# Performance work log

Measured on AMD Instinct MI355X. Metric: run time of the kernel, lower is better.

Reference implementation:

```python
import jax, jax.numpy as jnp
import numpy as np

NUM_HEADS = 16
HEAD_DIM = 64
MODEL_DIM = NUM_HEADS * HEAD_DIM  # 1024
N_TOKENS = 121
BATCH = 1024
DISTURB_HEADS = np.array([0, 3], dtype=int)


def setup_inputs() -> dict:
    key = jax.random.key(0)
    ks = jax.random.split(key, 8)
    scale = 1.0 / np.sqrt(MODEL_DIM)
    return {
        "query": jax.random.normal(ks[0], (BATCH, MODEL_DIM), dtype=jnp.float32),
        "key": jax.random.normal(ks[1], (BATCH, N_TOKENS, MODEL_DIM), dtype=jnp.float32),
        "value": jax.random.normal(ks[2], (BATCH, N_TOKENS, MODEL_DIM), dtype=jnp.float32),
        "Wq": jax.random.normal(ks[3], (MODEL_DIM, MODEL_DIM), dtype=jnp.float32) * scale,
        "bq": jnp.zeros((MODEL_DIM,), dtype=jnp.float32),
        "Wk": jax.random.normal(ks[4], (MODEL_DIM, MODEL_DIM), dtype=jnp.float32) * scale,
        "bk": jnp.zeros((MODEL_DIM,), dtype=jnp.float32),
        "Wv": jax.random.normal(ks[5], (MODEL_DIM, MODEL_DIM), dtype=jnp.float32) * scale,
        "bv": jnp.zeros((MODEL_DIM,), dtype=jnp.float32),
    }


def reference(query, key, value, Wq, bq, Wk, bk, Wv, bv):
    B, N, _ = key.shape
    H, d = NUM_HEADS, HEAD_DIM
    # Linear projections (plain GEMMs)
    q_proj = query @ Wq + bq            # [B, H*d]
    k_proj = key @ Wk + bk              # [B, N, H*d]
    v_proj = value @ Wv + bv            # [B, N, H*d]

    q = q_proj.reshape(B, H, d)         # [B, H, d]
    k = k_proj.reshape(B, N, H, d)      # [B, N, H, d]
    v = v_proj.reshape(B, N, H, d)

    # single-query scores per head: [B, H, N]
    scores = jnp.einsum('bhd,bnhd->bhn', q, k)
    # head-wise disturb override: masked heads get all-ones scores
    mask = jnp.zeros((H,), dtype=bool).at[DISTURB_HEADS].set(True)[None, :, None]
    scores = jnp.where(mask, jnp.ones_like(scores), scores)
    # note: original scales by sqrt(d * H), not sqrt(d)
    scores = scores / jnp.sqrt(jnp.asarray(d * H, dtype=scores.dtype))
    weights = jax.nn.softmax(scores, axis=-1)   # [B, H, N]
    output = jnp.einsum('bhn,bnhd->bhd', weights, v).reshape(B, H * d)
    return (output, weights)
```

## Files before the change

### kernel.cpp

```cpp
#include <hip/hip_runtime.h>
#include <hip/hip_bf16.h>

#define NHEADS 16
#define HDIM   64
#define MDIM   1024
#define NTOK   121
#define NBATCH 1024

typedef __attribute__((ext_vector_type(4))) float f32x4;
typedef __attribute__((ext_vector_type(4))) short s16x4;
typedef __attribute__((ext_vector_type(8))) short s16x8;

#define WAIT_VM(n)  asm volatile("s_waitcnt vmcnt(" #n ")" ::: "memory")
#define WAIT_LGKM0() asm volatile("s_waitcnt lgkmcnt(0)" ::: "memory")

__device__ __forceinline__ short f2bf(float f) {
  __hip_bfloat16 h = __float2bfloat16(f);
  return __builtin_bit_cast(short, h);
}

#define GLDS(gptr, lptr)                                                        \
  __builtin_amdgcn_global_load_lds(                                             \
      (const __attribute__((address_space(1))) void*)(gptr),                    \
      (__attribute__((address_space(3))) void*)(lptr), 16, 0, 0)

__global__ __launch_bounds__(256) void kTransW(const float* __restrict__ Wq,
                                               const float* __restrict__ Wk,
                                               const float* __restrict__ Wv,
                                               short* __restrict__ Wt) {
  int bid = blockIdx.x;
  int m = bid >> 8, tile = bid & 255;
  int tr = tile >> 4, tc = tile & 15;
  const float* W = (m == 0) ? Wq : (m == 1) ? Wk : Wv;
  short* T = Wt + (size_t)m * (MDIM * MDIM);
  __shared__ float tl[64][68];
  int t = threadIdx.x;
  int c4 = t & 15, r0 = t >> 4;
#pragma unroll
  for (int i = 0; i < 4; ++i) {
    int kr = r0 + i * 16;
    f32x4 v = *(const f32x4*)(W + (size_t)(tr * 64 + kr) * MDIM + tc * 64 + c4 * 4);
    *(f32x4*)&tl[kr][c4 * 4] = v;
  }
  __syncthreads();
#pragma unroll
  for (int i = 0; i < 4; ++i) {
    int n = r0 + i * 16;
    s16x4 o;
    o.x = f2bf(tl[c4 * 4 + 0][n]);
    o.y = f2bf(tl[c4 * 4 + 1][n]);
    o.z = f2bf(tl[c4 * 4 + 2][n]);
    o.w = f2bf(tl[c4 * 4 + 3][n]);
    *(s16x4*)(T + (size_t)(tc * 64 + n) * MDIM + tr * 64 + c4 * 4) = o;
  }
}

__device__ __forceinline__ void gemm_core(const float* __restrict__ A, int mrows,
                                          const short* __restrict__ Wt, int c0,
                                          short* Alds, short* Bl0, short* Bl1,
                                          f32x4 acc[4][4], int t) {
  int wid = t >> 6, lane = t & 63;
  int wr = wid >> 1, wc = wid & 1;
  int li = lane & 15, lg = lane >> 4;
  int kq = t & 15, r0s = t >> 4;
#pragma unroll
  for (int fm = 0; fm < 4; ++fm)
#pragma unroll
    for (int fn = 0; fn < 4; ++fn) acc[fm][fn] = (f32x4)0.0f;

  int rhi[4];
#pragma unroll
  for (int i = 0; i < 4; ++i) {
    int row = r0s + 64 + (i << 4);
    rhi[i] = row < mrows ? row : mrows - 1;
  }
#pragma unroll
  for (int i = 0; i < 4; ++i) {
    int cl = wid * 32 + i * 8 + (lane >> 3);
    int jg = (lane & 7) ^ (cl & 7);
    GLDS(Wt + (size_t)(c0 + cl) * MDIM + jg * 8, Bl0 + (wid * 32 + i * 8) * 64);
  }
  f32x4 rLo[4];
#pragma unroll
  for (int i = 0; i < 4; ++i)
    rLo[i] = *(const f32x4*)(A + (size_t)(r0s + (i << 4)) * MDIM + kq * 4);

  for (int kt = 0; kt < 16; ++kt) {
    int k0 = kt * 64;
    short* Bcur = (kt & 1) ? Bl1 : Bl0;
    short* Bnxt = (kt & 1) ? Bl0 : Bl1;
    int kn = (kt < 15) ? k0 + 64 : 0;

    f32x4 rHi[4];
#pragma unroll
    for (int i = 0; i < 4; ++i)
      rHi[i] = *(const f32x4*)(A + (size_t)rhi[i] * MDIM + k0 + kq * 4);

    WAIT_VM(4);
    __builtin_amdgcn_s_barrier();
#pragma unroll
    for (int i = 0; i < 4; ++i) {
      int row = r0s + (i << 4);
      s16x4 b4;
      b4.x = f2bf(rLo[i].x); b4.y = f2bf(rLo[i].y);
      b4.z = f2bf(rLo[i].z); b4.w = f2bf(rLo[i].w);
      int byte = (row * 128 + kq * 8) ^ ((row & 7) << 4);
      *(s16x4*)((char*)Alds + byte) = b4;
    }
#pragma unroll
    for (int i = 0; i < 4; ++i) {
      int cl = wid * 32 + i * 8 + (lane >> 3);
      int jg = (lane & 7) ^ (cl & 7);
      GLDS(Wt + (size_t)(c0 + cl) * MDIM + kn + jg * 8, Bnxt + (wid * 32 + i * 8) * 64);
    }
    WAIT_VM(4);
#pragma unroll
    for (int i = 0; i < 4; ++i) {
      int row = r0s + 64 + (i << 4);
      s16x4 b4;
      b4.x = f2bf(rHi[i].x); b4.y = f2bf(rHi[i].y);
      b4.z = f2bf(rHi[i].z); b4.w = f2bf(rHi[i].w);
      int byte = (row * 128 + kq * 8) ^ ((row & 7) << 4);
      *(s16x4*)((char*)Alds + byte) = b4;
    }
#pragma unroll
    for (int i = 0; i < 4; ++i)
      rLo[i] = *(const f32x4*)(A + (size_t)(r0s + (i << 4)) * MDIM + kn + kq * 4);

    WAIT_LGKM0();
    __builtin_amdgcn_s_barrier();
#pragma unroll
    for (int ks = 0; ks < 2; ++ks) {
      s16x8 af[4];
      int kb = ks * 64 + lg * 16;
#pragma unroll
      for (int fm = 0; fm < 4; ++fm) {
        int row = wr * 64 + fm * 16 + li;
        int byte = (row * 128 + kb) ^ ((row & 7) << 4);
        af[fm] = *(s16x8*)((char*)Alds + byte);
      }
#pragma unroll
      for (int fn = 0; fn < 4; ++fn) {
        int col = wc * 64 + fn * 16 + li;
        int byte = (col * 128 + kb) ^ ((col & 7) << 4);
        s16x8 bfv = *(s16x8*)((char*)Bcur + byte);
#pragma unroll
        for (int fm = 0; fm < 4; ++fm)
          acc[fm][fn] = __builtin_amdgcn_mfma_f32_16x16x32_bf16(af[fm], bfv,
                                                                acc[fm][fn], 0, 0, 0);
      }
    }
  }
}

__global__ __launch_bounds__(256, 3) void kQProj(const float* __restrict__ query,
                                                 const short* __restrict__ WtQ,
                                                 const float* __restrict__ bq,
                                                 float* __restrict__ qp) {
  __shared__ alignas(16) short Alds[128 * 64];
  __shared__ alignas(16) short Bl0[128 * 64];
  __shared__ alignas(16) short Bl1[128 * 64];
  int bid = blockIdx.x;
  int rt = bid >> 3, ct = bid & 7;
  f32x4 acc[4][4];
  int t = threadIdx.x;
  gemm_core(query + (size_t)rt * 128 * MDIM, 128, WtQ, ct * 128, Alds, Bl0, Bl1, acc, t);
  int wid = t >> 6, lane = t & 63;
  int wr = wid >> 1, wc = wid & 1, li = lane & 15, lg = lane >> 4;
#pragma unroll
  for (int fn = 0; fn < 4; ++fn) {
    int col = ct * 128 + wc * 64 + fn * 16 + li;
    float bqv = bq[col];
#pragma unroll
    for (int fm = 0; fm < 4; ++fm)
#pragma unroll
      for (int rr = 0; rr < 4; ++rr) {
        int row = rt * 128 + wr * 64 + fm * 16 + lg * 4 + rr;
        qp[(size_t)row * MDIM + col] = acc[fm][fn][rr] + bqv;
      }
  }
}

__global__ __launch_bounds__(256, 3) void kG(const float* __restrict__ qp,
                                             const short* __restrict__ WtK,
                                             short* __restrict__ g) {
  __shared__ alignas(16) short Alds[128 * 64];
  __shared__ alignas(16) short Blds[128 * 64];
  int bid = blockIdx.x;
  int h = bid >> 6, bt = (bid >> 3) & 7, it = bid & 7;
  int t = threadIdx.x;
  int wid = t >> 6, lane = t & 63;
  int wr = wid >> 1, wc = wid & 1, li = lane & 15, lg = lane >> 4;
  int kq = t & 15, r0s = t >> 4;
#pragma unroll
  for (int i = 0; i < 8; ++i) {
    int r = r0s + 16 * i;
    f32x4 v = *(const f32x4*)(qp + (size_t)(bt * 128 + r) * MDIM + h * 64 + kq * 4);
    s16x4 b4;
    b4.x = f2bf(v.x); b4.y = f2bf(v.y); b4.z = f2bf(v.z); b4.w = f2bf(v.w);
    int byte = (r * 128 + kq * 8) ^ ((r & 7) << 4);
    *(s16x4*)((char*)Alds + byte) = b4;
  }
  {
    int jr = t >> 2, qc = t & 3;
#pragma unroll
    for (int q = 0; q < 4; ++q) {
      s16x8 v = *(const s16x8*)(WtK + (size_t)(h * 64 + jr) * MDIM + it * 128 +
                                qc * 32 + q * 8);
#pragma unroll
      for (int e = 0; e < 8; ++e) {
        int i = qc * 32 + q * 8 + e;
        int byte = (i * 128 + jr * 2) ^ ((i & 7) << 4);
        *(short*)((char*)Blds + byte) = v[e];
      }
    }
  }
  __syncthreads();
  f32x4 acc[4][4];
#pragma unroll
  for (int fm = 0; fm < 4; ++fm)
#pragma unroll
    for (int fn = 0; fn < 4; ++fn) acc[fm][fn] = (f32x4)0.0f;
#pragma unroll
  for (int ks = 0; ks < 2; ++ks) {
    int kb = ks * 64 + lg * 16;
    s16x8 af[4];
#pragma unroll
    for (int fm = 0; fm < 4; ++fm) {
      int row = wr * 64 + fm * 16 + li;
      int byte = (row * 128 + kb) ^ ((row & 7) << 4);
      af[fm] = *(s16x8*)((char*)Alds + byte);
    }
#pragma unroll
    for (int fn = 0; fn < 4; ++fn) {
      int col = wc * 64 + fn * 16 + li;
      int byte = (col * 128 + kb) ^ ((col & 7) << 4);
      s16x8 bfv = *(s16x8*)((char*)Blds + byte);
#pragma unroll
      for (int fm = 0; fm < 4; ++fm)
        acc[fm][fn] = __builtin_amdgcn_mfma_f32_16x16x32_bf16(af[fm], bfv,
                                                              acc[fm][fn], 0, 0, 0);
    }
  }
#pragma unroll
  for (int fm = 0; fm < 4; ++fm)
#pragma unroll
    for (int rr = 0; rr < 4; ++rr) {
      int b = bt * 128 + wr * 64 + fm * 16 + lg * 4 + rr;
      short* gp = g + ((size_t)b * 16 + h) * 1024 + it * 128;
#pragma unroll
      for (int fn = 0; fn < 4; ++fn)
        gp[wc * 64 + fn * 16 + li] = f2bf(acc[fm][fn][rr]);
    }
}

__global__ __launch_bounds__(512) void kWV(const float* __restrict__ key,
                                           const float* __restrict__ value,
                                           const short* __restrict__ g,
                                           float* __restrict__ weights,
                                           short* __restrict__ vbar) {
  __shared__ alignas(16) short Kl0[128 * 64];
  __shared__ alignas(16) short Kl1[128 * 64];
  __shared__ alignas(16) short Glds[16 * 1024];
  __shared__ float s_lds[16][132];
  int b = blockIdx.x;
  int t = threadIdx.x;
  int wid = t >> 6, lane = t & 63, li = lane & 15, lg = lane >> 4;
  int kq = t & 15, r0s = t >> 4;
  int rcl[4];
#pragma unroll
  for (int i = 0; i < 4; ++i) {
    int r = r0s + 32 * i;
    rcl[i] = r < NTOK ? r : NTOK - 1;
  }
  const float* A = key + (size_t)b * NTOK * MDIM;
  const short* gb = g + (size_t)b * 16384;
#pragma unroll
  for (int q = 0; q < 4; ++q) {
    int c = q * 512 + t;
    s16x8 v = *(const s16x8*)(gb + c * 8);
    int byte = ((c >> 7) * 2048 + (c & 127) * 16) ^ (((c >> 7) & 7) << 4);
    *(s16x8*)((char*)Glds + byte) = v;
  }
  f32x4 rA0[4], rA1[4];
#pragma unroll
  for (int i = 0; i < 4; ++i)
    rA0[i] = *(const f32x4*)(A + (size_t)rcl[i] * MDIM + kq * 4);
#pragma unroll
  for (int i = 0; i < 4; ++i)
    rA1[i] = *(const f32x4*)(A + (size_t)rcl[i] * MDIM + 64 + kq * 4);
  WAIT_LGKM0();
  __builtin_amdgcn_s_barrier();
  f32x4 acc = (f32x4)0.0f;

  for (int kt = 0; kt < 16; kt += 2) {
    WAIT_VM(4);
#pragma unroll
    for (int i = 0; i < 4; ++i) {
      int row = r0s + 32 * i;
      s16x4 b4;
      b4.x = f2bf(rA0[i].x); b4.y = f2bf(rA0[i].y);
      b4.z = f2bf(rA0[i].z); b4.w = f2bf(rA0[i].w);
      int byte = (row * 128 + kq * 8) ^ ((row & 7) << 4);
      *(s16x4*)((char*)Kl0 + byte) = b4;
    }
    {
      int kn = (kt + 2 < 16) ? (kt + 2) * 64 : 0;
#pragma unroll
      for (int i = 0; i < 4; ++i)
        rA0[i] = *(const f32x4*)(A + (size_t)rcl[i] * MDIM + kn + kq * 4);
    }
    WAIT_LGKM0();
    __builtin_amdgcn_s_barrier();
#pragma unroll
    for (int ks = 0; ks < 2; ++ks) {
      int kb = ks * 64 + lg * 16;
      int row = wid * 16 + li;
      s16x8 af = *(s16x8*)((char*)Kl0 + ((row * 128 + kb) ^ ((row & 7) << 4)));
      int kel = kt * 64 + ks * 32 + lg * 8;
      s16x8 bf = *(s16x8*)((char*)Glds + ((li * 2048 + kel * 2) ^ ((li & 7) << 4)));
      acc = __builtin_amdgcn_mfma_f32_16x16x32_bf16(af, bf, acc, 0, 0, 0);
    }
    WAIT_VM(4);
#pragma unroll
    for (int i = 0; i < 4; ++i) {
      int row = r0s + 32 * i;
      s16x4 b4;
      b4.x = f2bf(rA1[i].x); b4.y = f2bf(rA1[i].y);
      b4.z = f2bf(rA1[i].z); b4.w = f2bf(rA1[i].w);
      int byte = (row * 128 + kq * 8) ^ ((row & 7) << 4);
      *(s16x4*)((char*)Kl1 + byte) = b4;
    }
    {
      int kn = (kt + 3 < 16) ? (kt + 3) * 64 : 64;
#pragma unroll
      for (int i = 0; i < 4; ++i)
        rA1[i] = *(const f32x4*)(A + (size_t)rcl[i] * MDIM + kn + kq * 4);
    }
    WAIT_LGKM0();
    __builtin_amdgcn_s_barrier();
#pragma unroll
    for (int ks = 0; ks < 2; ++ks) {
      int kb = ks * 64 + lg * 16;
      int row = wid * 16 + li;
      s16x8 af = *(s16x8*)((char*)Kl1 + ((row * 128 + kb) ^ ((row & 7) << 4)));
      int kel = (kt + 1) * 64 + ks * 32 + lg * 8;
      s16x8 bf = *(s16x8*)((char*)Glds + ((li * 2048 + kel * 2) ^ ((li & 7) << 4)));
      acc = __builtin_amdgcn_mfma_f32_16x16x32_bf16(af, bf, acc, 0, 0, 0);
    }
  }
#pragma unroll
  for (int rr = 0; rr < 4; ++rr) s_lds[li][wid * 16 + lg * 4 + rr] = acc[rr];
  __syncthreads();
  float (*w_lds)[128] = (float(*)[128])Glds;
#pragma unroll
  for (int hh = 0; hh < 2; ++hh) {
    int h = wid * 2 + hh;
    int n0 = lane, n1 = lane + 64;
    bool v0 = (n0 < NTOK), v1 = (n1 < NTOK);
    float w0, w1;
    if (h == 0 || h == 3) {
      w0 = 1.f / NTOK; w1 = 1.f / NTOK;
    } else {
      const float kinv = 1.f / 32.f;
      float s0 = v0 ? s_lds[h][n0] * kinv : -1e30f;
      float s1 = v1 ? s_lds[h][n1] * kinv : -1e30f;
      float m = fmaxf(s0, s1);
#pragma unroll
      for (int msk = 1; msk < 64; msk <<= 1) m = fmaxf(m, __shfl_xor(m, msk));
      float e0 = v0 ? __expf(s0 - m) : 0.f;
      float e1 = v1 ? __expf(s1 - m) : 0.f;
      float s = e0 + e1;
#pragma unroll
      for (int msk = 1; msk < 64; msk <<= 1) s += __shfl_xor(s, msk);
      float inv = 1.f / s;
      w0 = e0 * inv; w1 = e1 * inv;
    }
    float* wp = weights + ((size_t)b * NHEADS + h) * NTOK;
    if (v0) { wp[n0] = w0; w_lds[h][n0] = w0; }
    if (v1) { wp[n1] = w1; w_lds[h][n1] = w1; }
  }
  __syncthreads();

  int grp = t >> 7, ic = t & 127;
  const float* V = value + (size_t)b * NTOK * MDIM;
  f32x4 a0[4], a1[4];
#pragma unroll
  for (int hh = 0; hh < 4; ++hh) { a0[hh] = (f32x4)0.0f; a1[hh] = (f32x4)0.0f; }
#pragma unroll 4
  for (int n = 0; n < NTOK; ++n) {
    f32x4 v0 = *(const f32x4*)(V + (size_t)n * MDIM + ic * 8);
    f32x4 v1 = *(const f32x4*)(V + (size_t)n * MDIM + ic * 8 + 4);
#pragma unroll
    for (int hh = 0; hh < 4; ++hh) {
      float wn = w_lds[grp * 4 + hh][n];
      a0[hh] += wn * v0;
      a1[hh] += wn * v1;
    }
  }
#pragma unroll
  for (int hh = 0; hh < 4; ++hh) {
    s16x8 o;
    o[0] = f2bf(a0[hh].x); o[1] = f2bf(a0[hh].y);
    o[2] = f2bf(a0[hh].z); o[3] = f2bf(a0[hh].w);
    o[4] = f2bf(a1[hh].x); o[5] = f2bf(a1[hh].y);
    o[6] = f2bf(a1[hh].z); o[7] = f2bf(a1[hh].w);
    *(s16x8*)(vbar + ((size_t)b * 16 + grp * 4 + hh) * 1024 + ic * 8) = o;
  }
}

__global__ __launch_bounds__(256, 3) void kO(const short* __restrict__ vbar,
                                             const short* __restrict__ WtV,
                                             const float* __restrict__ bv,
                                             float* __restrict__ outp) {
  __shared__ alignas(16) short Alds[128 * 64];
  __shared__ alignas(16) short Blds[64 * 64];
  int bid = blockIdx.x;
  int bt = bid >> 4, h = bid & 15;
  int t = threadIdx.x;
  int wid = t >> 6, lane = t & 63;
  int wr = wid >> 1, wc = wid & 1, li = lane & 15, lg = lane >> 4;
  f32x4 acc[4][2];
#pragma unroll
  for (int fm = 0; fm < 4; ++fm)
#pragma unroll
    for (int fn = 0; fn < 2; ++fn) acc[fm][fn] = (f32x4)0.0f;

  for (int kt = 0; kt < 16; ++kt) {
    int k0 = kt * 64;
    __syncthreads();
#pragma unroll
    for (int i = 0; i < 4; ++i) {
      int lrow = wid * 32 + i * 8 + (lane >> 3);
      int jg = (lane & 7) ^ (lrow & 7);
      GLDS(vbar + ((size_t)(bt * 128 + lrow) * 16 + h) * 1024 + k0 + jg * 8,
           Alds + (wid * 32 + i * 8) * 64);
    }
#pragma unroll
    for (int j = 0; j < 2; ++j) {
      int cl = wid * 16 + j * 8 + (lane >> 3);
      int jg = (lane & 7) ^ (cl & 7);
      GLDS(WtV + (size_t)(h * 64 + cl) * MDIM + k0 + jg * 8,
           Blds + (wid * 16 + j * 8) * 64);
    }
    __syncthreads();
#pragma unroll
    for (int ks = 0; ks < 2; ++ks) {
      int kb = ks * 64 + lg * 16;
      s16x8 af[4];
#pragma unroll
      for (int fm = 0; fm < 4; ++fm) {
        int row = wr * 64 + fm * 16 + li;
        int byte = (row * 128 + kb) ^ ((row & 7) << 4);
        af[fm] = *(s16x8*)((char*)Alds + byte);
      }
#pragma unroll
      for (int fn = 0; fn < 2; ++fn) {
        int col = wc * 32 + fn * 16 + li;
        int byte = (col * 128 + kb) ^ ((col & 7) << 4);
        s16x8 bfv = *(s16x8*)((char*)Blds + byte);
#pragma unroll
        for (int fm = 0; fm < 4; ++fm)
          acc[fm][fn] = __builtin_amdgcn_mfma_f32_16x16x32_bf16(af[fm], bfv,
                                                                acc[fm][fn], 0, 0, 0);
      }
    }
  }
#pragma unroll
  for (int fn = 0; fn < 2; ++fn) {
    int cg = h * 64 + wc * 32 + fn * 16 + li;
    float bvv = bv[cg];
#pragma unroll
    for (int fm = 0; fm < 4; ++fm)
#pragma unroll
      for (int rr = 0; rr < 4; ++rr) {
        int row = bt * 128 + wr * 64 + fm * 16 + lg * 4 + rr;
        outp[(size_t)row * MDIM + cg] = acc[fm][fn][rr] + bvv;
      }
  }
}

extern "C" void kernel_launch(void* const* d_in, const int* in_sizes, int n_in,
                              void* d_out, int out_size, void* d_ws, size_t ws_size,
                              hipStream_t stream) {
  const float* query = (const float*)d_in[0];
  const float* key   = (const float*)d_in[1];
  const float* value = (const float*)d_in[2];
  const float* Wq    = (const float*)d_in[3];
  const float* bq    = (const float*)d_in[4];
  const float* Wk    = (const float*)d_in[5];
  const float* bk    = (const float*)d_in[6];
  const float* Wv    = (const float*)d_in[7];
  const float* bv    = (const float*)d_in[8];
  (void)bk;

  float* out     = (float*)d_out;
  float* weights = out + (size_t)NBATCH * MDIM;

  char* ws = (char*)d_ws;
  short* Wt   = (short*)ws;
  float* qp   = (float*)(ws + 6u  * 1024 * 1024);
  short* g    = (short*)(ws + 10u * 1024 * 1024);
  short* vbar = (short*)(ws + 48u * 1024 * 1024);

  kTransW<<<dim3(768),  dim3(256), 0, stream>>>(Wq, Wk, Wv, Wt);
  kQProj <<<dim3(64),   dim3(256), 0, stream>>>(query, Wt, bq, qp);
  kG     <<<dim3(1024), dim3(256), 0, stream>>>(qp, Wt + (size_t)MDIM * MDIM, g);
  kWV    <<<dim3(1024), dim3(512), 0, stream>>>(key, value, g, weights, vbar);
  kO     <<<dim3(128),  dim3(256), 0, stream>>>(vbar, Wt + 2 * (size_t)MDIM * MDIM,
                                                bv, out);
}
```

Baseline: 315.0 us.

## Store G in MFMA fragment order and read it directly, dropping LDS staging

kG now writes the projected query-key matrix G in the per-lane MFMA B-fragment layout, so kWV loads each fragment straight from global memory into registers. This removes the 32KB Glds buffer, its staging loads, and a barrier from kWV. With less LDS in use, launch bounds are raised so more blocks fit per CU. The cost is scattered 2-byte stores in kG and per-iteration global loads that the MFMA loop has to wait on. Zero padding is also added to w_lds for token indices past 121.

```diff
diff --git a/kernel.cpp b/kernel.cpp
--- a/kernel.cpp
+++ b/kernel.cpp
@@ -183,7 +183,7 @@
 
 __global__ __launch_bounds__(256, 3) void kG(const float* __restrict__ qp,
                                              const short* __restrict__ WtK,
-                                             short* __restrict__ g) {
+                                             short* __restrict__ g2) {
   __shared__ alignas(16) short Alds[128 * 64];
   __shared__ alignas(16) short Blds[128 * 64];
   int bid = blockIdx.x;
@@ -246,23 +246,27 @@
   for (int fm = 0; fm < 4; ++fm)
 #pragma unroll
     for (int rr = 0; rr < 4; ++rr) {
-      int b = bt * 128 + wr * 64 + fm * 16 + lg * 4 + rr;
-      short* gp = g + ((size_t)b * 16 + h) * 1024 + it * 128;
-#pragma unroll
-      for (int fn = 0; fn < 4; ++fn)
-        gp[wc * 64 + fn * 16 + li] = f2bf(acc[fm][fn][rr]);
-    }
-}
-
-__global__ __launch_bounds__(512) void kWV(const float* __restrict__ key,
-                                           const float* __restrict__ value,
-                                           const short* __restrict__ g,
-                                           float* __restrict__ weights,
-                                           short* __restrict__ vbar) {
+      int brow = bt * 128 + wr * 64 + fm * 16 + lg * 4 + rr;
+#pragma unroll
+      for (int fn = 0; fn < 4; ++fn) {
+        int i = it * 128 + wc * 64 + fn * 16 + li;
+        int c = i >> 5;
+        int lanecode = h + 16 * ((i >> 3) & 3);
+        size_t addr = (((size_t)brow * 32 + c) * 64 + lanecode) * 8 + (i & 7);
+        g2[addr] = f2bf(acc[fm][fn][rr]);
+      }
+    }
+}
+
+__global__ __launch_bounds__(512, 6) void kWV(const float* __restrict__ key,
+                                              const float* __restrict__ value,
+                                              const short* __restrict__ g2,
+                                              float* __restrict__ weights,
+                                              short* __restrict__ vbar) {
   __shared__ alignas(16) short Kl0[128 * 64];
   __shared__ alignas(16) short Kl1[128 * 64];
-  __shared__ alignas(16) short Glds[16 * 1024];
   __shared__ float s_lds[16][132];
+  __shared__ float w_lds[16][128];
   int b = blockIdx.x;
   int t = threadIdx.x;
   int wid = t >> 6, lane = t & 63, li = lane & 15, lg = lane >> 4;
@@ -274,14 +278,7 @@
     rcl[i] = r < NTOK ? r : NTOK - 1;
   }
   const float* A = key + (size_t)b * NTOK * MDIM;
-  const short* gb = g + (size_t)b * 16384;
-#pragma unroll
-  for (int q = 0; q < 4; ++q) {
-    int c = q * 512 + t;
-    s16x8 v = *(const s16x8*)(gb + c * 8);
-    int byte = ((c >> 7) * 2048 + (c & 127) * 16) ^ (((c >> 7) & 7) << 4);
-    *(s16x8*)((char*)Glds + byte) = v;
-  }
+  const short* g2b = g2 + (size_t)b * 16384;
   f32x4 rA0[4], rA1[4];
 #pragma unroll
   for (int i = 0; i < 4; ++i)
@@ -289,8 +286,6 @@
 #pragma unroll
   for (int i = 0; i < 4; ++i)
     rA1[i] = *(const f32x4*)(A + (size_t)rcl[i] * MDIM + 64 + kq * 4);
-  WAIT_LGKM0();
-  __builtin_amdgcn_s_barrier();
   f32x4 acc = (f32x4)0.0f;
 
   for (int kt = 0; kt < 16; kt += 2) {
@@ -304,6 +299,8 @@
       int byte = (row * 128 + kq * 8) ^ ((row & 7) << 4);
       *(s16x4*)((char*)Kl0 + byte) = b4;
     }
+    s16x8 bf0 = *(const s16x8*)(g2b + ((2 * kt + 0) * 64 + lane) * 8);
+    s16x8 bf1 = *(const s16x8*)(g2b + ((2 * kt + 1) * 64 + lane) * 8);
     {
       int kn = (kt + 2 < 16) ? (kt + 2) * 64 : 0;
 #pragma unroll
@@ -312,14 +309,12 @@
     }
     WAIT_LGKM0();
     __builtin_amdgcn_s_barrier();
-#pragma unroll
-    for (int ks = 0; ks < 2; ++ks) {
-      int kb = ks * 64 + lg * 16;
+    {
       int row = wid * 16 + li;
-      s16x8 af = *(s16x8*)((char*)Kl0 + ((row * 128 + kb) ^ ((row & 7) << 4)));
-      int kel = kt * 64 + ks * 32 + lg * 8;
-      s16x8 bf = *(s16x8*)((char*)Glds + ((li * 2048 + kel * 2) ^ ((li & 7) << 4)));
-      acc = __builtin_amdgcn_mfma_f32_16x16x32_bf16(af, bf, acc, 0, 0, 0);
+      s16x8 af0 = *(s16x8*)((char*)Kl0 + ((row * 128 + lg * 16) ^ ((row & 7) << 4)));
+      acc = __builtin_amdgcn_mfma_f32_16x16x32_bf16(af0, bf0, acc, 0, 0, 0);
+      s16x8 af1 = *(s16x8*)((char*)Kl0 + ((row * 128 + 64 + lg * 16) ^ ((row & 7) << 4)));
+      acc = __builtin_amdgcn_mfma_f32_16x16x32_bf16(af1, bf1, acc, 0, 0, 0);
     }
     WAIT_VM(4);
 #pragma unroll
@@ -331,6 +326,8 @@
       int byte = (row * 128 + kq * 8) ^ ((row & 7) << 4);
       *(s16x4*)((char*)Kl1 + byte) = b4;
     }
+    s16x8 bf2 = *(const s16x8*)(g2b + ((2 * kt + 2) * 64 + lane) * 8);
+    s16x8 bf3 = *(const s16x8*)(g2b + ((2 * kt + 3) * 64 + lane) * 8);
     {
       int kn = (kt + 3 < 16) ? (kt + 3) * 64 : 64;
 #pragma unroll
@@ -339,20 +336,17 @@
     }
     WAIT_LGKM0();
     __builtin_amdgcn_s_barrier();
-#pragma unroll
-    for (int ks = 0; ks < 2; ++ks) {
-      int kb = ks * 64 + lg * 16;
+    {
       int row = wid * 16 + li;
-      s16x8 af = *(s16x8*)((char*)Kl1 + ((row * 128 + kb) ^ ((row & 7) << 4)));
-      int kel = (kt + 1) * 64 + ks * 32 + lg * 8;
-      s16x8 bf = *(s16x8*)((char*)Glds + ((li * 2048 + kel * 2) ^ ((li & 7) << 4)));
-      acc = __builtin_amdgcn_mfma_f32_16x16x32_bf16(af, bf, acc, 0, 0, 0);
+      s16x8 af0 = *(s16x8*)((char*)Kl1 + ((row * 128 + lg * 16) ^ ((row & 7) << 4)));
+      acc = __builtin_amdgcn_mfma_f32_16x16x32_bf16(af0, bf2, acc, 0, 0, 0);
+      s16x8 af1 = *(s16x8*)((char*)Kl1 + ((row * 128 + 64 + lg * 16) ^ ((row & 7) << 4)));
+      acc = __builtin_amdgcn_mfma_f32_16x16x32_bf16(af1, bf3, acc, 0, 0, 0);
     }
   }
 #pragma unroll
   for (int rr = 0; rr < 4; ++rr) s_lds[li][wid * 16 + lg * 4 + rr] = acc[rr];
   __syncthreads();
-  float (*w_lds)[128] = (float(*)[128])Glds;
 #pragma unroll
   for (int hh = 0; hh < 2; ++hh) {
     int h = wid * 2 + hh;
@@ -379,6 +373,7 @@
     float* wp = weights + ((size_t)b * NHEADS + h) * NTOK;
     if (v0) { wp[n0] = w0; w_lds[h][n0] = w0; }
     if (v1) { wp[n1] = w1; w_lds[h][n1] = w1; }
+    if (lane < 7) w_lds[h][NTOK + lane] = 0.f;
   }
   __syncthreads();
 
@@ -500,13 +495,13 @@
   char* ws = (char*)d_ws;
   short* Wt   = (short*)ws;
   float* qp   = (float*)(ws + 6u  * 1024 * 1024);
-  short* g    = (short*)(ws + 10u * 1024 * 1024);
+  short* g2   = (short*)(ws + 10u * 1024 * 1024);
   short* vbar = (short*)(ws + 48u * 1024 * 1024);
 
   kTransW<<<dim3(768),  dim3(256), 0, stream>>>(Wq, Wk, Wv, Wt);
   kQProj <<<dim3(64),   dim3(256), 0, stream>>>(query, Wt, bq, qp);
-  kG     <<<dim3(1024), dim3(256), 0, stream>>>(qp, Wt + (size_t)MDIM * MDIM, g);
-  kWV    <<<dim3(1024), dim3(512), 0, stream>>>(key, value, g, weights, vbar);
+  kG     <<<dim3(1024), dim3(256), 0, stream>>>(qp, Wt + (size_t)MDIM * MDIM, g2);
+  kWV    <<<dim3(1024), dim3(512), 0, stream>>>(key, value, g2, weights, vbar);
   kO     <<<dim3(128),  dim3(256), 0, stream>>>(vbar, Wt + 2 * (size_t)MDIM * MDIM,
                                                 bv, out);
 }
```

Result: slower. 552.9 us (+75.5%).
